# Kernel tuning notes

Hardware: AMD Instinct MI355X
Metric: run time of the kernel (lower is better)

The kernel has to match this reference:

```python
import jax, jax.numpy as jnp
import numpy as np

IN_ = 64
FEATURE = 1024
BATCH = 256

def setup_inputs() -> dict:
    key = jax.random.key(0)
    kx, kw = jax.random.split(key)
    x = jax.random.normal(kx, (BATCH, IN_, FEATURE), dtype=jnp.float32)
    # W[i] corresponds to torch Linear weight of shape [out_features, in_features]
    # scaled like torch's default kaiming-uniform-ish init (bound = 1/sqrt(fan_in))
    bound = 1.0 / np.sqrt(FEATURE)
    W = jax.random.uniform(kw, (IN_, FEATURE, FEATURE), dtype=jnp.float32,
                           minval=-bound, maxval=bound)
    return {"x": x, "W": W}

def reference(x, W):
    # Per-position independent linear: out[b,i,o] = sum_f x[b,i,f] * W[i,o,f]
    # (torch Linear computes x @ W^T). Single batched GEMM via einsum.
    return jnp.einsum('bif,iof->bio', x, W)
```

## Files before the change

### kernel.cpp

```cpp
#include <hip/hip_runtime.h>
#include <hip/hip_bf16.h>

#define IN_CNT 64
#define FEAT   1024
#define BATCH  256

#define BM 256
#define BN 256
#define BK 32
#define KT (FEAT / BK)

typedef __attribute__((ext_vector_type(4))) float f32x4;
typedef __attribute__((ext_vector_type(8))) short bf16x8;

__device__ __forceinline__ short f2bf(float f) {
    __hip_bfloat16 h = __float2bfloat16(f);
    return __builtin_bit_cast(short, h);
}

__device__ __forceinline__ bf16x8 pack8(f32x4 a, f32x4 b) {
    bf16x8 v;
    v[0] = f2bf(a[0]); v[1] = f2bf(a[1]); v[2] = f2bf(a[2]); v[3] = f2bf(a[3]);
    v[4] = f2bf(b[0]); v[5] = f2bf(b[1]); v[6] = f2bf(b[2]); v[7] = f2bf(b[3]);
    return v;
}

__device__ __forceinline__ void barrier_lgkm() {
    asm volatile("s_waitcnt lgkmcnt(0)" ::: "memory");
    __builtin_amdgcn_s_barrier();
    asm volatile("" ::: "memory");
}

__device__ __forceinline__ void gload16(const float* g, float* l) {
    __builtin_amdgcn_global_load_lds(
        (const __attribute__((address_space(1))) void*)g,
        (__attribute__((address_space(3))) void*)l, 16, 0, 0);
}

__global__ __launch_bounds__(512, 2)
void split_linear_kernel(const float* __restrict__ x,
                         const float* __restrict__ W,
                         float* __restrict__ out)
{
    __shared__ __align__(16) float lds[32768];

    const int tid = threadIdx.x;

    const int bid = blockIdx.x;
    const int swz = ((bid & 7) << 5) | (bid >> 3);
    const int gi   = swz >> 2;
    const int ncol = (swz & 3) << 8;

    const int lane = tid & 63;
    const int wid  = tid >> 6;
    const int wm   = wid >> 2;
    const int wn   = wid & 3;
    const int lr   = lane & 15;
    const int lh   = lane >> 4;

    const int lrow = lane >> 3;
    const int lgr  = (lane & 7) ^ lrow;
    const float* Asrc = x + ((size_t)lrow * IN_CNT + gi) * FEAT + lgr * 4;
    const float* Bsrc = W + ((size_t)gi * FEAT + ncol + lrow) * FEAT + lgr * 4;

    f32x4 acc[8][4];
#pragma unroll
    for (int m = 0; m < 8; ++m)
#pragma unroll
        for (int n = 0; n < 4; ++n)
            acc[m][n] = (f32x4){0.f, 0.f, 0.f, 0.f};

    auto ISSUE = [&](int kt, int b) {
        float* base = lds + b * 16384;
        const float* a0 = Asrc + (size_t)kt * BK;
        const float* b0 = Bsrc + (size_t)kt * BK;
#pragma unroll
        for (int i = 0; i < 4; ++i) {
            const int c = wid * 4 + i;
            gload16(a0 + (size_t)c * (8 * IN_CNT * FEAT), base + c * 256);
            gload16(b0 + (size_t)c * (8 * FEAT),          base + 8192 + c * 256);
        }
    };

    const int sl0 = ((2 * lh)     ^ (lr & 7)) << 2;
    const int sl1 = ((2 * lh + 1) ^ (lr & 7)) << 2;

    auto COMPUTE = [&](int b) {
        const float* bufA = lds + b * 16384;
        const float* bufB = bufA + 8192;
        bf16x8 bfr[4];
#pragma unroll
        for (int nf = 0; nf < 4; ++nf) {
            const float* rp = bufB + (wn * 64 + nf * 16 + lr) * 32;
            bfr[nf] = pack8(*(const f32x4*)(rp + sl0), *(const f32x4*)(rp + sl1));
        }
#pragma unroll
        for (int mf = 0; mf < 8; ++mf) {
            const float* rp = bufA + (wm * 128 + mf * 16 + lr) * 32;
            bf16x8 af = pack8(*(const f32x4*)(rp + sl0), *(const f32x4*)(rp + sl1));
#pragma unroll
            for (int nf = 0; nf < 4; ++nf)
                acc[mf][nf] = __builtin_amdgcn_mfma_f32_16x16x32_bf16(
                    af, bfr[nf], acc[mf][nf], 0, 0, 0);
        }
    };

    ISSUE(0, 0);
    ISSUE(1, 1);
    asm volatile("s_waitcnt vmcnt(8)" ::: "memory");
    __builtin_amdgcn_s_barrier();
    asm volatile("" ::: "memory");

    for (int k = 0; k < KT; ++k) {
        const int b = k & 1;
        COMPUTE(b);
        barrier_lgkm();
        if (k + 2 < KT) {
            ISSUE(k + 2, b);
            asm volatile("s_waitcnt vmcnt(8)" ::: "memory");
        } else {
            asm volatile("s_waitcnt vmcnt(0)" ::: "memory");
        }
        __builtin_amdgcn_s_barrier();
        asm volatile("" ::: "memory");
    }

#define ELD 260
    float* elds = lds;
#pragma unroll
    for (int s = 0; s < 4; ++s) {
        barrier_lgkm();
        if (wm == (s >> 1)) {
            const int mfb = (s & 1) * 4;
#pragma unroll
            for (int f = 0; f < 4; ++f)
#pragma unroll
                for (int nf = 0; nf < 4; ++nf)
#pragma unroll
                    for (int j = 0; j < 4; ++j)
                        elds[(f * 16 + lh * 4 + j) * ELD + wn * 64 + nf * 16 + lr]
                            = acc[mfb + f][nf][j];
        }
        barrier_lgkm();
#pragma unroll
        for (int rr = 0; rr < 8; ++rr) {
            const int rowl = wid * 8 + rr;
            f32x4 v = *(const f32x4*)&elds[rowl * ELD + lane * 4];
            const int m = s * 64 + rowl;
            *(f32x4*)&out[((size_t)m * IN_CNT + gi) * FEAT + ncol + lane * 4] = v;
        }
    }
#undef ELD
}

extern "C" void kernel_launch(void* const* d_in, const int* in_sizes, int n_in,
                              void* d_out, int out_size, void* d_ws, size_t ws_size,
                              hipStream_t stream) {
    const float* x   = (const float*)d_in[0];
    const float* W   = (const float*)d_in[1];
    float*       out = (float*)d_out;

    dim3 grid(IN_CNT * (FEAT / BN));
    dim3 block(512);
    hipLaunchKernelGGL(split_linear_kernel, grid, block, 0, stream, x, W, out);
}
```

Baseline: 94.72 us.

## Split A/B staging and interleave loads with half-tile MFMA phases

Splits the combined tile load into separate A and B stages. The next A tile is now issued before the first half of the MFMA work, and the B tile two steps ahead is issued after the mid-iteration barrier, once B fragments are already in registers. This lets B's LDS buffer be refilled while the second half of the MFMAs runs. MFMA phases are wrapped in s_setprio to favour matrix issue. The aim is to overlap global-to-LDS traffic with compute more evenly and to shorten the prefetch depth for A. The cost is more complex vmcnt accounting and less lookahead for A.

After: 94.19 us. No clear change (-0.6%).

```diff
diff --git a/kernel.cpp b/kernel.cpp
--- a/kernel.cpp
+++ b/kernel.cpp
@@ -70,32 +70,42 @@
         for (int n = 0; n < 4; ++n)
             acc[m][n] = (f32x4){0.f, 0.f, 0.f, 0.f};
 
-    auto ISSUE = [&](int kt, int b) {
-        float* base = lds + b * 16384;
+    auto STAGE_A = [&](int kt, int bb) {
+        float* base = lds + bb * 16384;
         const float* a0 = Asrc + (size_t)kt * BK;
+#pragma unroll
+        for (int i = 0; i < 4; ++i) {
+            const int c = wid * 4 + i;
+            gload16(a0 + (size_t)c * (8 * IN_CNT * FEAT), base + c * 256);
+        }
+    };
+    auto STAGE_B = [&](int kt, int bb) {
+        float* base = lds + bb * 16384 + 8192;
         const float* b0 = Bsrc + (size_t)kt * BK;
 #pragma unroll
         for (int i = 0; i < 4; ++i) {
             const int c = wid * 4 + i;
-            gload16(a0 + (size_t)c * (8 * IN_CNT * FEAT), base + c * 256);
-            gload16(b0 + (size_t)c * (8 * FEAT),          base + 8192 + c * 256);
+            gload16(b0 + (size_t)c * (8 * FEAT), base + c * 256);
         }
     };
 
     const int sl0 = ((2 * lh)     ^ (lr & 7)) << 2;
     const int sl1 = ((2 * lh + 1) ^ (lr & 7)) << 2;
 
-    auto COMPUTE = [&](int b) {
-        const float* bufA = lds + b * 16384;
-        const float* bufB = bufA + 8192;
-        bf16x8 bfr[4];
+    bf16x8 bfr[4];
+    auto READ_B = [&](int bb) {
+        const float* bufB = lds + bb * 16384 + 8192;
 #pragma unroll
         for (int nf = 0; nf < 4; ++nf) {
             const float* rp = bufB + (wn * 64 + nf * 16 + lr) * 32;
             bfr[nf] = pack8(*(const f32x4*)(rp + sl0), *(const f32x4*)(rp + sl1));
         }
+    };
+    auto MFMA_HALF = [&](int bb, int ph) {
+        const float* bufA = lds + bb * 16384;
 #pragma unroll
-        for (int mf = 0; mf < 8; ++mf) {
+        for (int m4 = 0; m4 < 4; ++m4) {
+            const int mf = ph * 4 + m4;
             const float* rp = bufA + (wm * 128 + mf * 16 + lr) * 32;
             bf16x8 af = pack8(*(const f32x4*)(rp + sl0), *(const f32x4*)(rp + sl1));
 #pragma unroll
@@ -105,19 +115,27 @@
         }
     };
 
-    ISSUE(0, 0);
-    ISSUE(1, 1);
-    asm volatile("s_waitcnt vmcnt(8)" ::: "memory");
+    STAGE_B(0, 0);
+    STAGE_A(0, 0);
+    STAGE_B(1, 1);
+    asm volatile("s_waitcnt vmcnt(4)" ::: "memory");
     __builtin_amdgcn_s_barrier();
     asm volatile("" ::: "memory");
 
-    for (int k = 0; k < KT; ++k) {
-        const int b = k & 1;
-        COMPUTE(b);
+    for (int t = 0; t < KT; ++t) {
+        const int bb = t & 1;
+        READ_B(bb);
+        if (t + 1 < KT) STAGE_A(t + 1, bb ^ 1);
+        __builtin_amdgcn_s_setprio(1);
+        MFMA_HALF(bb, 0);
+        __builtin_amdgcn_s_setprio(0);
         barrier_lgkm();
-        if (k + 2 < KT) {
-            ISSUE(k + 2, b);
-            asm volatile("s_waitcnt vmcnt(8)" ::: "memory");
+        if (t + 2 < KT) STAGE_B(t + 2, bb);
+        __builtin_amdgcn_s_setprio(1);
+        MFMA_HALF(bb, 1);
+        __builtin_amdgcn_s_setprio(0);
+        if (t + 2 < KT) {
+            asm volatile("s_waitcnt vmcnt(4)" ::: "memory");
         } else {
             asm volatile("s_waitcnt vmcnt(0)" ::: "memory");
         }
```
